# Kernel tuning notes

Measured on AMD Instinct MI355X. Metric: run time of the kernel, lower is better.

The kernel has to match this reference:

```python
import jax, jax.numpy as jnp
import numpy as np

N_QUBITS = 8
N_LAYERS = 3
B = 32768
IN_F = 512
OUT_F = 512


def _apply_1q(state, G, q):
    # state: (B, 2,...,2) complex64; G: (2,2) shared or (B,2,2) per-sample gate
    s = jnp.moveaxis(state, 1 + q, -1)
    if G.ndim == 3:
        s = jnp.einsum('bij,...j->...i'.replace('...', 'b...').replace('b...ij', 'bij'), G, s) if False else jnp.einsum('bij,b...j->b...i', G, s)
    else:
        s = jnp.einsum('ij,b...j->b...i', G, s)
    return jnp.moveaxis(s, -1, 1 + q)


def _cnot(state, c, t):
    # flip target axis on the control=1 slice
    ca, ta = 1 + c, 1 + t
    s0 = jax.lax.index_in_dim(state, 0, ca, keepdims=True)
    s1 = jax.lax.index_in_dim(state, 1, ca, keepdims=True)
    s1 = jnp.flip(s1, axis=ta)
    return jnp.concatenate([s0, s1], axis=ca)


def _circuit(angles, qparams):
    # angles: (B, 8) RY embedding angles; qparams: (3, 8) RX layer angles
    b = angles.shape[0]
    state = jnp.zeros((b, 2 ** N_QUBITS), dtype=jnp.complex64).at[:, 0].set(1.0)
    state = state.reshape((b,) + (2,) * N_QUBITS)
    # RY(theta) = [[c, -s], [s, c]], per-sample angles
    half = 0.5 * angles
    c, s = jnp.cos(half), jnp.sin(half)
    for q in range(N_QUBITS):
        G = jnp.stack([jnp.stack([c[:, q], -s[:, q]], -1),
                       jnp.stack([s[:, q], c[:, q]], -1)], -2).astype(jnp.complex64)
        state = _apply_1q(state, G, q)
    # layers: RX(params[l,q]) on each wire, then ring of CNOTs
    hp = 0.5 * qparams
    cp, sp = jnp.cos(hp), jnp.sin(hp)
    for l in range(N_LAYERS):
        for q in range(N_QUBITS):
            # RX(theta) = [[c, -i s], [-i s, c]]
            G = jnp.stack([jnp.stack([cp[l, q] + 0j, -1j * sp[l, q]], -1),
                           jnp.stack([-1j * sp[l, q], cp[l, q] + 0j], -1)], -2).astype(jnp.complex64)
            state = _apply_1q(state, G, q)
        for i in range(N_QUBITS - 1):
            state = _cnot(state, i, i + 1)
        state = _cnot(state, N_QUBITS - 1, 0)
    # <Z_q> = P(bit_q=0) - P(bit_q=1)
    probs = jnp.real(state) ** 2 + jnp.imag(state) ** 2
    zs = []
    for q in range(N_QUBITS):
        p = jnp.moveaxis(probs, 1 + q, 1).reshape(b, 2, -1).sum(-1)
        zs.append(p[:, 0] - p[:, 1])
    return jnp.stack(zs, axis=1)  # (B, 8) float32


def setup_inputs() -> dict:
    key = jax.random.key(0)
    k = jax.random.split(key, 6)
    x = jax.random.normal(k[0], (B, IN_F), dtype=jnp.float32)
    fc_w = jax.random.normal(k[1], (N_QUBITS, IN_F), dtype=jnp.float32) / np.sqrt(IN_F)
    fc_b = jax.random.normal(k[2], (N_QUBITS,), dtype=jnp.float32) * 0.01
    qparams = jax.random.normal(k[3], (N_LAYERS, N_QUBITS), dtype=jnp.float32) * 0.1
    post_w = jax.random.normal(k[4], (OUT_F, N_QUBITS), dtype=jnp.float32) / np.sqrt(N_QUBITS)
    post_b = jax.random.normal(k[5], (OUT_F,), dtype=jnp.float32) * 0.01
    return {"x": x, "fc_w": fc_w, "fc_b": fc_b, "qparams": qparams,
            "post_w": post_w, "post_b": post_b}


def reference(x, fc_w, fc_b, qparams, post_w, post_b):
    xproj = x @ fc_w.T + fc_b            # (B, 8) angles
    z = _circuit(xproj, qparams)          # (B, 8) PauliZ expectations
    return z @ post_w.T + post_b          # (B, OUT_F)
```

## Files before the change

kernel.cpp:

```cpp
#include <hip/hip_runtime.h>

#define BLOCK 512
typedef float v2f __attribute__((ext_vector_type(2)));

__device__ __forceinline__ v2f pk_fma(v2f a, v2f b, v2f c) {
  v2f d;
  asm("v_pk_fma_f32 %0, %1, %2, %3" : "=v"(d) : "v"(a), "v"(b), "v"(c));
  return d;
}
__device__ __forceinline__ v2f pk_mul_swap(v2f s, v2f p) {
  v2f d;
  asm("v_pk_mul_f32 %0, %1, %2 op_sel:[0,1] op_sel_hi:[1,0]" : "=v"(d) : "v"(s), "v"(p));
  return d;
}

template<int CTRL>
__device__ __forceinline__ float dpp_f(float v) {
  return __int_as_float(__builtin_amdgcn_mov_dpp(__float_as_int(v), CTRL, 0xF, 0xF, true));
}
template<int MASK>
__device__ __forceinline__ float shx(float v) {
  if constexpr (MASK == 1)      return dpp_f<0xB1>(v);
  else if constexpr (MASK == 2) return dpp_f<0x4E>(v);
  else if constexpr (MASK == 8) return dpp_f<0x128>(v);
  else
    return __int_as_float(__builtin_amdgcn_ds_swizzle(__float_as_int(v), 0x101F));
}

template<int CTRL, int BANK>
__device__ __forceinline__ void cnot_dpp(v2f& a) {
  a.x = __int_as_float(__builtin_amdgcn_update_dpp(
      __float_as_int(a.x), __float_as_int(a.x), CTRL, 0xF, BANK, false));
  a.y = __int_as_float(__builtin_amdgcn_update_dpp(
      __float_as_int(a.y), __float_as_int(a.y), CTRL, 0xF, BANK, false));
}

__device__ __forceinline__ v2f cmul(v2f A, v2f B) {
  v2f d;
  d.x = __builtin_fmaf(A.x, B.x, -(A.y * B.y));
  d.y = __builtin_fmaf(A.x, B.y,  (A.y * B.x));
  return d;
}
__device__ __forceinline__ void swap_v(v2f& a, v2f& b) { v2f t = a; a = b; b = t; }

__global__ __launch_bounds__(BLOCK, 8) void qcnn_kernel(
    const float* __restrict__ x,   const float* __restrict__ fcw,
    const float* __restrict__ fcb, const float* __restrict__ qp,
    const float* __restrict__ pw,  const float* __restrict__ pb,
    float* __restrict__ out)
{
  __shared__ float s_fcw[8 * 512];
  __shared__ float s_pwt[8 * 512];
  __shared__ float s_pb[512];
  __shared__ v2f   s_trig[3][8];

  const int tid = threadIdx.x;

#pragma unroll
  for (int i = tid; i < 1024; i += BLOCK)
    ((float4*)s_fcw)[i] = ((const float4*)fcw)[i];
#pragma unroll
  for (int i = tid; i < 4096; i += BLOCK)
    s_pwt[i] = pw[(i & 511) * 8 + (i >> 9)];
  if (tid < 128) ((float4*)s_pb)[tid] = ((const float4*)pb)[tid];
  if (tid < 24) {
    const float h = 0.5f * qp[tid];
    v2f cspair; cspair.x = __cosf(h); cspair.y = __sinf(h);
    s_trig[tid >> 3][tid & 7] = cspair;
  }
  __syncthreads();

  const int wave = tid >> 6;
  const int lane = tid & 63;
  const int u = lane & 15;
  const int g = lane >> 4;
  const int smp = (blockIdx.x * (BLOCK / 64) + wave) * 4 + g;

  const float* xrow = x + (size_t)smp * 512;
  v2f acc2[8];
#pragma unroll
  for (int q = 0; q < 8; ++q) { acc2[q].x = 0.f; acc2[q].y = 0.f; }
#pragma unroll
  for (int t = 0; t < 8; ++t) {
    const float4 xv = *(const float4*)(xrow + u * 4 + t * 64);
    v2f x01; x01.x = xv.x; x01.y = xv.y;
    v2f x23; x23.x = xv.z; x23.y = xv.w;
#pragma unroll
    for (int q = 0; q < 8; ++q) {
      const float4 wv = *(const float4*)(s_fcw + q * 512 + u * 4 + t * 64);
      v2f w01; w01.x = wv.x; w01.y = wv.y;
      v2f w23; w23.x = wv.z; w23.y = wv.w;
      acc2[q] = pk_fma(x01, w01, acc2[q]);
      acc2[q] = pk_fma(x23, w23, acc2[q]);
    }
  }
  float cs[8], sn[8];
#pragma unroll
  for (int q = 0; q < 8; ++q) {
    float a_ = acc2[q].x + acc2[q].y;
    a_ += shx<1>(a_); a_ += shx<2>(a_); a_ += shx<4>(a_); a_ += shx<8>(a_);
    const float h = 0.5f * (a_ + fcb[q]);
    cs[q] = __cosf(h);
    sn[q] = __sinf(h);
  }

  v2f L;
  {
    v2f t0 = s_trig[0][0];
    const bool b0 = (u & 8) != 0;
    L.x =  t0.x * (b0 ? sn[0] : cs[0]);
    L.y = -t0.y * (b0 ? cs[0] : sn[0]);
    const int bits[3] = {2, 4, 1};
#pragma unroll
    for (int q = 1; q < 4; ++q) {
      v2f tq = s_trig[0][q];
      const bool b = (u & bits[q - 1]) != 0;
      v2f v;
      v.x =  tq.x * (b ? sn[q] : cs[q]);
      v.y = -tq.y * (b ? cs[q] : sn[q]);
      L = cmul(L, v);
    }
  }
  v2f A4[4], C4[4];
#pragma unroll
  for (int j = 0; j < 4; ++j) {
    const int q = 4 + j;
    v2f tq = s_trig[0][q];
    A4[j].x =  tq.x * cs[q];  A4[j].y = -tq.y * sn[q];
    C4[j].x =  tq.x * sn[q];  C4[j].y = -tq.y * cs[q];
  }
  v2f p45[4], p67[4];
#pragma unroll
  for (int i = 0; i < 4; ++i) {
    p45[i] = cmul((i & 2) ? C4[0] : A4[0], (i & 1) ? C4[1] : A4[1]);
    p67[i] = cmul((i & 2) ? C4[2] : A4[2], (i & 1) ? C4[3] : A4[3]);
  }
  v2f Lp[4];
#pragma unroll
  for (int i = 0; i < 4; ++i) Lp[i] = cmul(L, p45[i]);
  v2f a[16];
#pragma unroll
  for (int r = 0; r < 16; ++r) a[r] = cmul(Lp[r >> 2], p67[r & 3]);

  const bool cn12 = (u & 2) != 0;
  const bool cn34 = (u & 1) != 0;
#pragma unroll
  for (int l = 0; l < 3; ++l) {
    if (l > 0) {
      {
        v2f tq = s_trig[l][0];
        const float c = tq.x;
        v2f ss; ss.x = tq.y; ss.y = -tq.y;
        v2f cc; cc.x = c; cc.y = c;
#pragma unroll
        for (int r = 0; r < 16; ++r) {
          v2f psw;
          psw.x = shx<8>(a[r].y);
          psw.y = shx<8>(a[r].x);
          v2f t; asm("v_pk_mul_f32 %0, %1, %2" : "=v"(t) : "v"(ss), "v"(psw));
          a[r] = pk_fma(cc, a[r], t);
        }
      }
      {
        v2f tq = s_trig[l][1];
        v2f ss; ss.x = tq.y; ss.y = -tq.y;
        v2f cc; cc.x = tq.x; cc.y = tq.x;
#pragma unroll
        for (int r = 0; r < 16; ++r) {
          v2f psw; psw.x = shx<2>(a[r].y); psw.y = shx<2>(a[r].x);
          v2f t; asm("v_pk_mul_f32 %0, %1, %2" : "=v"(t) : "v"(ss), "v"(psw));
          a[r] = pk_fma(cc, a[r], t);
        }
      }
      {
        v2f tq = s_trig[l][2];
        v2f ss; ss.x = tq.y; ss.y = -tq.y;
        v2f cc; cc.x = tq.x; cc.y = tq.x;
#pragma unroll
        for (int r = 0; r < 16; ++r) {
          v2f psw; psw.x = shx<4>(a[r].y); psw.y = shx<4>(a[r].x);
          v2f t; asm("v_pk_mul_f32 %0, %1, %2" : "=v"(t) : "v"(ss), "v"(psw));
          a[r] = pk_fma(cc, a[r], t);
        }
      }
      {
        v2f tq = s_trig[l][3];
        v2f ss; ss.x = tq.y; ss.y = -tq.y;
        v2f cc; cc.x = tq.x; cc.y = tq.x;
#pragma unroll
        for (int r = 0; r < 16; ++r) {
          v2f psw; psw.x = shx<1>(a[r].y); psw.y = shx<1>(a[r].x);
          v2f t; asm("v_pk_mul_f32 %0, %1, %2" : "=v"(t) : "v"(ss), "v"(psw));
          a[r] = pk_fma(cc, a[r], t);
        }
      }
      {
        const int RM[4] = {8, 4, 2, 1};
#pragma unroll
        for (int j = 0; j < 4; ++j) {
          v2f tq = s_trig[l][4 + j];
          v2f ss; ss.x = tq.y; ss.y = -tq.y;
          v2f cc; cc.x = tq.x; cc.y = tq.x;
#pragma unroll
          for (int r = 0; r < 16; ++r) {
            if (!(r & RM[j])) {
              const int r1 = r | RM[j];
              v2f tlo = pk_mul_swap(ss, a[r1]);
              v2f thi = pk_mul_swap(ss, a[r]);
              a[r]  = pk_fma(cc, a[r],  tlo);
              a[r1] = pk_fma(cc, a[r1], thi);
            }
          }
        }
      }
    }
#pragma unroll
    for (int r = 0; r < 16; ++r) cnot_dpp<0x4E, 0xC>(a[r]);
#pragma unroll
    for (int r = 0; r < 16; ++r) {
      const float sx = shx<4>(a[r].x);
      const float sy = shx<4>(a[r].y);
      a[r].x = cn12 ? sx : a[r].x;
      a[r].y = cn12 ? sy : a[r].y;
    }
#pragma unroll
    for (int r = 0; r < 16; ++r) cnot_dpp<0xB1, 0xA>(a[r]);
#pragma unroll
    for (int r = 0; r < 8; ++r) {
      const v2f lo = a[r], hi = a[r + 8];
      a[r].x = cn34 ? hi.x : lo.x;  a[r].y = cn34 ? hi.y : lo.y;
      a[r + 8].x = cn34 ? lo.x : hi.x;  a[r + 8].y = cn34 ? lo.y : hi.y;
    }
    swap_v(a[8], a[12]);  swap_v(a[9], a[13]);  swap_v(a[10], a[14]); swap_v(a[11], a[15]);
    swap_v(a[4], a[6]);   swap_v(a[5], a[7]);   swap_v(a[12], a[14]); swap_v(a[13], a[15]);
    swap_v(a[2], a[3]);   swap_v(a[6], a[7]);   swap_v(a[10], a[11]); swap_v(a[14], a[15]);
#pragma unroll
    for (int r = 1; r < 16; r += 2) {
      a[r].x = shx<8>(a[r].x);
      a[r].y = shx<8>(a[r].y);
    }
  }

  float p[16];
#pragma unroll
  for (int r = 0; r < 16; ++r) p[r] = __builtin_fmaf(a[r].x, a[r].x, a[r].y * a[r].y);
  float e0[8], d7 = 0.f;
#pragma unroll
  for (int k = 0; k < 8; ++k) { e0[k] = p[2*k] + p[2*k+1]; d7 += p[2*k] - p[2*k+1]; }
  float e1[4], d6 = 0.f;
#pragma unroll
  for (int k = 0; k < 4; ++k) { e1[k] = e0[2*k] + e0[2*k+1]; d6 += e0[2*k] - e0[2*k+1]; }
  float e2[2], d5 = 0.f;
#pragma unroll
  for (int k = 0; k < 2; ++k) { e2[k] = e1[2*k] + e1[2*k+1]; d5 += e1[2*k] - e1[2*k+1]; }
  float S  = e2[0] + e2[1];
  float d4 = e2[0] - e2[1];

  float t;
  t = shx<1>(S);  float d3 = S - t;  S += t;
  d4 += shx<1>(d4); d5 += shx<1>(d5); d6 += shx<1>(d6); d7 += shx<1>(d7);
  t = shx<2>(S);  float d2 = S - t;  S += t;
  d3 += shx<2>(d3); d4 += shx<2>(d4); d5 += shx<2>(d5); d6 += shx<2>(d6); d7 += shx<2>(d7);
  t = shx<4>(S);  float d1 = S - t;  S += t;
  d2 += shx<4>(d2); d3 += shx<4>(d3); d4 += shx<4>(d4); d5 += shx<4>(d5); d6 += shx<4>(d6); d7 += shx<4>(d7);
  t = shx<8>(S);  float d0 = S - t;
  d1 += shx<8>(d1); d2 += shx<8>(d2); d3 += shx<8>(d3); d4 += shx<8>(d4); d5 += shx<8>(d5); d6 += shx<8>(d6); d7 += shx<8>(d7);

  float z[8];
  z[0] = (u & 8) ? -d0 : d0;
  z[1] = (u & 2) ? -d2 : d2;
  z[2] = (u & 4) ? -d1 : d1;
  z[3] = (u & 1) ? -d3 : d3;
  z[4] = d4; z[5] = d5; z[6] = d6; z[7] = d7;

  v2f zz[8];
#pragma unroll
  for (int q = 0; q < 8; ++q) { zz[q].x = z[q]; zz[q].y = z[q]; }
  float* orow = out + (size_t)smp * 512;
#pragma unroll
  for (int tt = 0; tt < 8; ++tt) {
    const int o = u * 4 + tt * 64;
    const float4 pbv = *(const float4*)(s_pb + o);
    v2f r0; r0.x = pbv.x; r0.y = pbv.y;
    v2f r1; r1.x = pbv.z; r1.y = pbv.w;
#pragma unroll
    for (int q = 0; q < 8; ++q) {
      const float4 wv = *(const float4*)(s_pwt + q * 512 + o);
      v2f w01; w01.x = wv.x; w01.y = wv.y;
      v2f w23; w23.x = wv.z; w23.y = wv.w;
      r0 = pk_fma(zz[q], w01, r0);
      r1 = pk_fma(zz[q], w23, r1);
    }
    float4 ov; ov.x = r0.x; ov.y = r0.y; ov.z = r1.x; ov.w = r1.y;
    *(float4*)(orow + o) = ov;
  }
}

extern "C" void kernel_launch(void* const* d_in, const int* in_sizes, int n_in,
                              void* d_out, int out_size, void* d_ws, size_t ws_size,
                              hipStream_t stream) {
  const float* x   = (const float*)d_in[0];
  const float* fcw = (const float*)d_in[1];
  const float* fcb = (const float*)d_in[2];
  const float* qp  = (const float*)d_in[3];
  const float* pw  = (const float*)d_in[4];
  const float* pb  = (const float*)d_in[5];
  float* out = (float*)d_out;

  dim3 grid(1024), block(BLOCK);
  hipLaunchKernelGGL(qcnn_kernel, grid, block, 0, stream, x, fcw, fcb, qp, pw, pb, out);
}
```

Before: 139.1 us.

## Replace statevector simulation with precomputed diagonal-phase kernel for Z expectations

```diff
diff --git a/kernel.cpp b/kernel.cpp
--- a/kernel.cpp
+++ b/kernel.cpp
@@ -6,6 +6,11 @@
 __device__ __forceinline__ v2f pk_fma(v2f a, v2f b, v2f c) {
   v2f d;
   asm("v_pk_fma_f32 %0, %1, %2, %3" : "=v"(d) : "v"(a), "v"(b), "v"(c));
+  return d;
+}
+__device__ __forceinline__ v2f pk_mul(v2f a, v2f b) {
+  v2f d;
+  asm("v_pk_mul_f32 %0, %1, %2" : "=v"(d) : "v"(a), "v"(b));
   return d;
 }
 __device__ __forceinline__ v2f pk_mul_swap(v2f s, v2f p) {
@@ -27,23 +32,27 @@
     return __int_as_float(__builtin_amdgcn_ds_swizzle(__float_as_int(v), 0x101F));
 }
 
-template<int CTRL, int BANK>
-__device__ __forceinline__ void cnot_dpp(v2f& a) {
-  a.x = __int_as_float(__builtin_amdgcn_update_dpp(
-      __float_as_int(a.x), __float_as_int(a.x), CTRL, 0xF, BANK, false));
-  a.y = __int_as_float(__builtin_amdgcn_update_dpp(
-      __float_as_int(a.y), __float_as_int(a.y), CTRL, 0xF, BANK, false));
-}
-
-__device__ __forceinline__ v2f cmul(v2f A, v2f B) {
-  v2f d;
-  d.x = __builtin_fmaf(A.x, B.x, -(A.y * B.y));
-  d.y = __builtin_fmaf(A.x, B.y,  (A.y * B.x));
-  return d;
-}
-__device__ __forceinline__ void swap_v(v2f& a, v2f& b) { v2f t = a; a = b; b = t; }
-
-__global__ __launch_bounds__(BLOCK, 8) void qcnn_kernel(
+__device__ __forceinline__ int gmap(int b) {
+#pragma unroll
+  for (int j = 0; j < 7; ++j) b ^= ((b >> (j + 1)) & 1) << j;
+  b ^= (b & 1) << 7;
+  return b;
+}
+
+__device__ __forceinline__ float dotK(const v2f* pp, const v2f* kcol) {
+  v2f a0; a0.x = 0.f; a0.y = 0.f;
+  v2f a1; a1.x = 0.f; a1.y = 0.f;
+#pragma unroll
+  for (int k = 0; k < 8; k += 2) {
+    a0 = pk_fma(pp[k],     kcol[k * 16],       a0);
+    a1 = pk_fma(pp[k + 1], kcol[(k + 1) * 16], a1);
+  }
+  return (a0.x + a1.x) + (a0.y + a1.y);
+}
+
+#define MQ_PACKED 0x99CC66B359AC5632ULL
+
+__global__ __launch_bounds__(BLOCK, 4) void qcnn_kernel(
     const float* __restrict__ x,   const float* __restrict__ fcw,
     const float* __restrict__ fcb, const float* __restrict__ qp,
     const float* __restrict__ pw,  const float* __restrict__ pb,
@@ -52,7 +61,8 @@
   __shared__ float s_fcw[8 * 512];
   __shared__ float s_pwt[8 * 512];
   __shared__ float s_pb[512];
-  __shared__ v2f   s_trig[3][8];
+  __shared__ float s_beta[256];
+  __shared__ v2f   s_K2[8][8][16];
 
   const int tid = threadIdx.x;
 
@@ -63,10 +73,29 @@
   for (int i = tid; i < 4096; i += BLOCK)
     s_pwt[i] = pw[(i & 511) * 8 + (i >> 9)];
   if (tid < 128) ((float4*)s_pb)[tid] = ((const float4*)pb)[tid];
-  if (tid < 24) {
-    const float h = 0.5f * qp[tid];
-    v2f cspair; cspair.x = __cosf(h); cspair.y = __sinf(h);
-    s_trig[tid >> 3][tid & 7] = cspair;
+
+  if (tid < 256) {
+    const int c = tid;
+    const int i1 = gmap(c);
+    const int i2 = gmap(i1);
+    float ang = 0.f;
+#pragma unroll
+    for (int q = 0; q < 8; ++q) {
+      ang += (((c  >> q) & 1) ? 0.5f : -0.5f) * qp[q];
+      ang += (((i1 >> q) & 1) ? 0.5f : -0.5f) * qp[8 + q];
+      ang += (((i2 >> q) & 1) ? 0.5f : -0.5f) * qp[16 + q];
+    }
+    s_beta[c] = ang;
+  }
+  __syncthreads();
+
+#pragma unroll
+  for (int i = tid; i < 2048; i += BLOCK) {
+    const int q = i >> 8, c = i & 255;
+    const int m = (int)((MQ_PACKED >> (8 * q)) & 0xFF);
+    const float kv = __cosf(s_beta[c ^ m] - s_beta[c]) * (1.0f / 256.0f);
+    const int uu = c >> 4, rr = c & 15;
+    ((float*)s_K2)[((q * 8 + (rr >> 1)) * 16 + uu) * 2 + (rr & 1)] = kv;
   }
   __syncthreads();
 
@@ -74,225 +103,128 @@
   const int lane = tid & 63;
   const int u = lane & 15;
   const int g = lane >> 4;
-  const int smp = (blockIdx.x * (BLOCK / 64) + wave) * 4 + g;
-
-  const float* xrow = x + (size_t)smp * 512;
-  v2f acc2[8];
-#pragma unroll
-  for (int q = 0; q < 8; ++q) { acc2[q].x = 0.f; acc2[q].y = 0.f; }
-#pragma unroll
-  for (int t = 0; t < 8; ++t) {
-    const float4 xv = *(const float4*)(xrow + u * 4 + t * 64);
-    v2f x01; x01.x = xv.x; x01.y = xv.y;
-    v2f x23; x23.x = xv.z; x23.y = xv.w;
+
+#pragma unroll 1
+  for (int tile = 0; tile < 2; ++tile) {
+    const int smp = blockIdx.x * 64 + tile * 32 + wave * 4 + g;
+
+    const float* xrow = x + (size_t)smp * 512;
+    v2f acc2[8];
+#pragma unroll
+    for (int q = 0; q < 8; ++q) { acc2[q].x = 0.f; acc2[q].y = 0.f; }
+#pragma unroll
+    for (int t = 0; t < 8; ++t) {
+      const float4 xv = *(const float4*)(xrow + u * 4 + t * 64);
+      v2f x01; x01.x = xv.x; x01.y = xv.y;
+      v2f x23; x23.x = xv.z; x23.y = xv.w;
+#pragma unroll
+      for (int q = 0; q < 8; ++q) {
+        const float4 wv = *(const float4*)(s_fcw + q * 512 + u * 4 + t * 64);
+        v2f w01; w01.x = wv.x; w01.y = wv.y;
+        v2f w23; w23.x = wv.z; w23.y = wv.w;
+        acc2[q] = pk_fma(x01, w01, acc2[q]);
+        acc2[q] = pk_fma(x23, w23, acc2[q]);
+      }
+    }
+    float th[8];
 #pragma unroll
     for (int q = 0; q < 8; ++q) {
-      const float4 wv = *(const float4*)(s_fcw + q * 512 + u * 4 + t * 64);
-      v2f w01; w01.x = wv.x; w01.y = wv.y;
-      v2f w23; w23.x = wv.z; w23.y = wv.w;
-      acc2[q] = pk_fma(x01, w01, acc2[q]);
-      acc2[q] = pk_fma(x23, w23, acc2[q]);
-    }
-  }
-  float cs[8], sn[8];
-#pragma unroll
-  for (int q = 0; q < 8; ++q) {
-    float a_ = acc2[q].x + acc2[q].y;
-    a_ += shx<1>(a_); a_ += shx<2>(a_); a_ += shx<4>(a_); a_ += shx<8>(a_);
-    const float h = 0.5f * (a_ + fcb[q]);
-    cs[q] = __cosf(h);
-    sn[q] = __sinf(h);
-  }
-
-  v2f L;
-  {
-    v2f t0 = s_trig[0][0];
-    const bool b0 = (u & 8) != 0;
-    L.x =  t0.x * (b0 ? sn[0] : cs[0]);
-    L.y = -t0.y * (b0 ? cs[0] : sn[0]);
-    const int bits[3] = {2, 4, 1};
-#pragma unroll
-    for (int q = 1; q < 4; ++q) {
-      v2f tq = s_trig[0][q];
-      const bool b = (u & bits[q - 1]) != 0;
-      v2f v;
-      v.x =  tq.x * (b ? sn[q] : cs[q]);
-      v.y = -tq.y * (b ? cs[q] : sn[q]);
-      L = cmul(L, v);
-    }
-  }
-  v2f A4[4], C4[4];
-#pragma unroll
-  for (int j = 0; j < 4; ++j) {
-    const int q = 4 + j;
-    v2f tq = s_trig[0][q];
-    A4[j].x =  tq.x * cs[q];  A4[j].y = -tq.y * sn[q];
-    C4[j].x =  tq.x * sn[q];  C4[j].y = -tq.y * cs[q];
-  }
-  v2f p45[4], p67[4];
-#pragma unroll
-  for (int i = 0; i < 4; ++i) {
-    p45[i] = cmul((i & 2) ? C4[0] : A4[0], (i & 1) ? C4[1] : A4[1]);
-    p67[i] = cmul((i & 2) ? C4[2] : A4[2], (i & 1) ? C4[3] : A4[3]);
-  }
-  v2f Lp[4];
-#pragma unroll
-  for (int i = 0; i < 4; ++i) Lp[i] = cmul(L, p45[i]);
-  v2f a[16];
-#pragma unroll
-  for (int r = 0; r < 16; ++r) a[r] = cmul(Lp[r >> 2], p67[r & 3]);
-
-  const bool cn12 = (u & 2) != 0;
-  const bool cn34 = (u & 1) != 0;
-#pragma unroll
-  for (int l = 0; l < 3; ++l) {
-    if (l > 0) {
-      {
-        v2f tq = s_trig[l][0];
-        const float c = tq.x;
-        v2f ss; ss.x = tq.y; ss.y = -tq.y;
-        v2f cc; cc.x = c; cc.y = c;
-#pragma unroll
-        for (int r = 0; r < 16; ++r) {
-          v2f psw;
-          psw.x = shx<8>(a[r].y);
-          psw.y = shx<8>(a[r].x);
-          v2f t; asm("v_pk_mul_f32 %0, %1, %2" : "=v"(t) : "v"(ss), "v"(psw));
-          a[r] = pk_fma(cc, a[r], t);
-        }
+      float a_ = acc2[q].x + acc2[q].y;
+      a_ += shx<1>(a_); a_ += shx<2>(a_); a_ += shx<4>(a_); a_ += shx<8>(a_);
+      th[q] = a_ + fcb[q];
+    }
+
+    float uf[8], vf[8];
+#pragma unroll
+    for (int q = 0; q < 8; ++q) {
+      const float h = 0.5f * th[q];
+      const float c_ = __cosf(h), s_ = __sinf(h);
+      uf[q] = c_ + s_; vf[q] = c_ - s_;
+    }
+    v2f wr2[8];
+    {
+      v2f P01; P01.x = uf[0]; P01.y = vf[0];
+      const float r12[4] = {uf[1] * uf[2], vf[1] * uf[2], uf[1] * vf[2], vf[1] * vf[2]};
+#pragma unroll
+      for (int k = 0; k < 8; ++k) {
+        const float rest = r12[k & 3] * ((k & 4) ? vf[3] : uf[3]);
+        v2f rr; rr.x = rest; rr.y = rest;
+        wr2[k] = pk_mul(P01, rr);
       }
-      {
-        v2f tq = s_trig[l][1];
-        v2f ss; ss.x = tq.y; ss.y = -tq.y;
-        v2f cc; cc.x = tq.x; cc.y = tq.x;
-#pragma unroll
-        for (int r = 0; r < 16; ++r) {
-          v2f psw; psw.x = shx<2>(a[r].y); psw.y = shx<2>(a[r].x);
-          v2f t; asm("v_pk_mul_f32 %0, %1, %2" : "=v"(t) : "v"(ss), "v"(psw));
-          a[r] = pk_fma(cc, a[r], t);
-        }
+    }
+    float wup[8];
+    {
+      const bool b4 = (u & 1), b5 = (u & 2), b6 = (u & 4), b7 = (u & 8);
+      const float f4 = b4 ? vf[4] : uf[4], g4 = b4 ? uf[4] : vf[4];
+      const float f5 = b5 ? vf[5] : uf[5], g5 = b5 ? uf[5] : vf[5];
+      const float f6 = b6 ? vf[6] : uf[6], g6 = b6 ? uf[6] : vf[6];
+      const float f7 = b7 ? vf[7] : uf[7], g7 = b7 ? uf[7] : vf[7];
+      const float A0 = f4 * f5, A1 = g4 * f5, A2 = f4 * g5, A3 = g4 * g5;
+      const float B0 = f6 * f7, B1 = g6 * f7, B2 = f6 * g7, B3 = g6 * g7;
+      const float wu = A0 * B0;
+      wup[0] = wu * (A3 * B0);
+      wup[1] = wu * (A1 * B1);
+      wup[2] = wu * (A2 * B2);
+      wup[3] = wup[1];
+      wup[4] = wu * (A3 * B2);
+      wup[5] = wu * (A2 * B1);
+      wup[6] = wu * (A0 * B3);
+      wup[7] = wu * (A1 * B2);
+    }
+
+    float zp[8];
+    {
+      const v2f* kb = (const v2f*)s_K2 + u;
+      v2f pp[8];
+#pragma unroll
+      for (int k = 0; k < 8; ++k) pp[k] = pk_mul(wr2[k], wr2[k ^ 1]);
+      zp[0] = dotK(pp, kb + 0 * 128) * wup[0];
+#pragma unroll
+      for (int k = 0; k < 8; ++k) pp[k] = pk_mul_swap(wr2[k], wr2[k ^ 1]);
+      zp[4] = dotK(pp, kb + 4 * 128) * wup[4];
+#pragma unroll
+      for (int k = 0; k < 8; ++k) pp[k] = pk_mul(wr2[k], wr2[k ^ 3]);
+      zp[1] = dotK(pp, kb + 1 * 128) * wup[1];
+      zp[5] = dotK(pp, kb + 5 * 128) * wup[5];
+#pragma unroll
+      for (int k = 0; k < 8; ++k) pp[k] = pk_mul(wr2[k], wr2[k ^ 6]);
+      zp[2] = dotK(pp, kb + 2 * 128) * wup[2];
+      zp[6] = dotK(pp, kb + 6 * 128) * wup[6];
+#pragma unroll
+      for (int k = 0; k < 8; ++k) pp[k] = pk_mul_swap(wr2[k], wr2[k ^ 4]);
+      zp[3] = dotK(pp, kb + 3 * 128) * wup[3];
+      zp[7] = dotK(pp, kb + 7 * 128) * wup[7];
+    }
+#pragma unroll
+    for (int q = 0; q < 8; ++q) zp[q] += shx<1>(zp[q]);
+#pragma unroll
+    for (int q = 0; q < 8; ++q) zp[q] += shx<2>(zp[q]);
+#pragma unroll
+    for (int q = 0; q < 8; ++q) zp[q] += shx<4>(zp[q]);
+#pragma unroll
+    for (int q = 0; q < 8; ++q) zp[q] += shx<8>(zp[q]);
+
+    v2f zz[8];
+#pragma unroll
+    for (int q = 0; q < 8; ++q) { zz[q].x = zp[q]; zz[q].y = zp[q]; }
+    float* orow = out + (size_t)smp * 512;
+#pragma unroll
+    for (int tt = 0; tt < 8; ++tt) {
+      const int o = u * 4 + tt * 64;
+      const float4 pbv = *(const float4*)(s_pb + o);
+      v2f r0; r0.x = pbv.x; r0.y = pbv.y;
+      v2f r1; r1.x = pbv.z; r1.y = pbv.w;
+#pragma unroll
+      for (int q = 0; q < 8; ++q) {
+        const float4 wv = *(const float4*)(s_pwt + q * 512 + o);
+        v2f w01; w01.x = wv.x; w01.y = wv.y;
+        v2f w23; w23.x = wv.z; w23.y = wv.w;
+        r0 = pk_fma(zz[q], w01, r0);
+        r1 = pk_fma(zz[q], w23, r1);
       }
-      {
-        v2f tq = s_trig[l][2];
-        v2f ss; ss.x = tq.y; ss.y = -tq.y;
-        v2f cc; cc.x = tq.x; cc.y = tq.x;
-#pragma unroll
-        for (int r = 0; r < 16; ++r) {
-          v2f psw; psw.x = shx<4>(a[r].y); psw.y = shx<4>(a[r].x);
-          v2f t; asm("v_pk_mul_f32 %0, %1, %2" : "=v"(t) : "v"(ss), "v"(psw));
-          a[r] = pk_fma(cc, a[r], t);
-        }
-      }
-      {
-        v2f tq = s_trig[l][3];
-        v2f ss; ss.x = tq.y; ss.y = -tq.y;
-        v2f cc; cc.x = tq.x; cc.y = tq.x;
-#pragma unroll
-        for (int r = 0; r < 16; ++r) {
-          v2f psw; psw.x = shx<1>(a[r].y); psw.y = shx<1>(a[r].x);
-          v2f t; asm("v_pk_mul_f32 %0, %1, %2" : "=v"(t) : "v"(ss), "v"(psw));
-          a[r] = pk_fma(cc, a[r], t);
-        }
-      }
-      {
-        const int RM[4] = {8, 4, 2, 1};
-#pragma unroll
-        for (int j = 0; j < 4; ++j) {
-          v2f tq = s_trig[l][4 + j];
-          v2f ss; ss.x = tq.y; ss.y = -tq.y;
-          v2f cc; cc.x = tq.x; cc.y = tq.x;
-#pragma unroll
-          for (int r = 0; r < 16; ++r) {
-            if (!(r & RM[j])) {
-              const int r1 = r | RM[j];
-              v2f tlo = pk_mul_swap(ss, a[r1]);
-              v2f thi = pk_mul_swap(ss, a[r]);
-              a[r]  = pk_fma(cc, a[r],  tlo);
-              a[r1] = pk_fma(cc, a[r1], thi);
-            }
-          }
-        }
-      }
-    }
-#pragma unroll
-    for (int r = 0; r < 16; ++r) cnot_dpp<0x4E, 0xC>(a[r]);
-#pragma unroll
-    for (int r = 0; r < 16; ++r) {
-      const float sx = shx<4>(a[r].x);
-      const float sy = shx<4>(a[r].y);
-      a[r].x = cn12 ? sx : a[r].x;
-      a[r].y = cn12 ? sy : a[r].y;
-    }
-#pragma unroll
-    for (int r = 0; r < 16; ++r) cnot_dpp<0xB1, 0xA>(a[r]);
-#pragma unroll
-    for (int r = 0; r < 8; ++r) {
-      const v2f lo = a[r], hi = a[r + 8];
-      a[r].x = cn34 ? hi.x : lo.x;  a[r].y = cn34 ? hi.y : lo.y;
-      a[r + 8].x = cn34 ? lo.x : hi.x;  a[r + 8].y = cn34 ? lo.y : hi.y;
-    }
-    swap_v(a[8], a[12]);  swap_v(a[9], a[13]);  swap_v(a[10], a[14]); swap_v(a[11], a[15]);
-    swap_v(a[4], a[6]);   swap_v(a[5], a[7]);   swap_v(a[12], a[14]); swap_v(a[13], a[15]);
-    swap_v(a[2], a[3]);   swap_v(a[6], a[7]);   swap_v(a[10], a[11]); swap_v(a[14], a[15]);
-#pragma unroll
-    for (int r = 1; r < 16; r += 2) {
-      a[r].x = shx<8>(a[r].x);
-      a[r].y = shx<8>(a[r].y);
-    }
-  }
-
-  float p[16];
-#pragma unroll
-  for (int r = 0; r < 16; ++r) p[r] = __builtin_fmaf(a[r].x, a[r].x, a[r].y * a[r].y);
-  float e0[8], d7 = 0.f;
-#pragma unroll
-  for (int k = 0; k < 8; ++k) { e0[k] = p[2*k] + p[2*k+1]; d7 += p[2*k] - p[2*k+1]; }
-  float e1[4], d6 = 0.f;
-#pragma unroll
-  for (int k = 0; k < 4; ++k) { e1[k] = e0[2*k] + e0[2*k+1]; d6 += e0[2*k] - e0[2*k+1]; }
-  float e2[2], d5 = 0.f;
-#pragma unroll
-  for (int k = 0; k < 2; ++k) { e2[k] = e1[2*k] + e1[2*k+1]; d5 += e1[2*k] - e1[2*k+1]; }
-  float S  = e2[0] + e2[1];
-  float d4 = e2[0] - e2[1];
-
-  float t;
-  t = shx<1>(S);  float d3 = S - t;  S += t;
-  d4 += shx<1>(d4); d5 += shx<1>(d5); d6 += shx<1>(d6); d7 += shx<1>(d7);
-  t = shx<2>(S);  float d2 = S - t;  S += t;
-  d3 += shx<2>(d3); d4 += shx<2>(d4); d5 += shx<2>(d5); d6 += shx<2>(d6); d7 += shx<2>(d7);
-  t = shx<4>(S);  float d1 = S - t;  S += t;
-  d2 += shx<4>(d2); d3 += shx<4>(d3); d4 += shx<4>(d4); d5 += shx<4>(d5); d6 += shx<4>(d6); d7 += shx<4>(d7);
-  t = shx<8>(S);  float d0 = S - t;
-  d1 += shx<8>(d1); d2 += shx<8>(d2); d3 += shx<8>(d3); d4 += shx<8>(d4); d5 += shx<8>(d5); d6 += shx<8>(d6); d7 += shx<8>(d7);
-
-  float z[8];
-  z[0] = (u & 8) ? -d0 : d0;
-  z[1] = (u & 2) ? -d2 : d2;
-  z[2] = (u & 4) ? -d1 : d1;
-  z[3] = (u & 1) ? -d3 : d3;
-  z[4] = d4; z[5] = d5; z[6] = d6; z[7] = d7;
-
-  v2f zz[8];
-#pragma unroll
-  for (int q = 0; q < 8; ++q) { zz[q].x = z[q]; zz[q].y = z[q]; }
-  float* orow = out + (size_t)smp * 512;
-#pragma unroll
-  for (int tt = 0; tt < 8; ++tt) {
-    const int o = u * 4 + tt * 64;
-    const float4 pbv = *(const float4*)(s_pb + o);
-    v2f r0; r0.x = pbv.x; r0.y = pbv.y;
-    v2f r1; r1.x = pbv.z; r1.y = pbv.w;
-#pragma unroll
-    for (int q = 0; q < 8; ++q) {
-      const float4 wv = *(const float4*)(s_pwt + q * 512 + o);
-      v2f w01; w01.x = wv.x; w01.y = wv.y;
-      v2f w23; w23.x = wv.z; w23.y = wv.w;
-      r0 = pk_fma(zz[q], w01, r0);
-      r1 = pk_fma(zz[q], w23, r1);
-    }
-    float4 ov; ov.x = r0.x; ov.y = r0.y; ov.z = r1.x; ov.w = r1.y;
-    *(float4*)(orow + o) = ov;
+      float4 ov; ov.x = r0.x; ov.y = r0.y; ov.z = r1.x; ov.w = r1.y;
+      *(float4*)(orow + o) = ov;
+    }
   }
 }
 
@@ -307,6 +239,6 @@
   const float* pb  = (const float*)d_in[5];
   float* out = (float*)d_out;
 
-  dim3 grid(1024), block(BLOCK);
+  dim3 grid(512), block(BLOCK);
   hipLaunchKernelGGL(qcnn_kernel, grid, block, 0, stream, x, fcw, fcb, qp, pw, pb, out);
 }
```

Result: faster. 134.5 us (-3.3%).
